# Performance work log

Hardware: AMD Instinct MI355X
Metric: run time of the kernel (lower is better)

## Reference

```python
import jax, jax.numpy as jnp
import numpy as np

B, N, D, H = 1, 512, 128, 128  # batch, seq, pair dim, hidden dim
EPS = 1e-6  # flax nnx LayerNorm default epsilon


def _layernorm(x, scale, bias):
    m = jnp.mean(x, axis=-1, keepdims=True)
    v = jnp.var(x, axis=-1, keepdims=True)
    return (x - m) * jax.lax.rsqrt(v + EPS) * scale + bias


def setup_inputs() -> dict:
    key = jax.random.key(0)
    ks = jax.random.split(key, 12)
    s = 0.02  # param init scale
    inp = {
        "x": jax.random.normal(ks[0], (B, N, N, D), jnp.float32),
        "src_mask": jnp.ones((B, N), jnp.float32),
        # first LayerNorm
        "ln1_scale": jnp.ones((D,), jnp.float32),
        "ln1_bias": jnp.zeros((D,), jnp.float32),
        # left/right projections
        "wl": jax.random.normal(ks[1], (D, H), jnp.float32) * s,
        "bl": jnp.zeros((H,), jnp.float32),
        "wr": jax.random.normal(ks[2], (D, H), jnp.float32) * s,
        "br": jnp.zeros((H,), jnp.float32),
        # gates (original inits kernel=0, bias=1; use small random kernels + bias=1 for a nontrivial baseline)
        "wlg": jax.random.normal(ks[3], (D, H), jnp.float32) * s,
        "blg": jnp.ones((H,), jnp.float32),
        "wrg": jax.random.normal(ks[4], (D, H), jnp.float32) * s,
        "brg": jnp.ones((H,), jnp.float32),
        "wog": jax.random.normal(ks[5], (D, H), jnp.float32) * s,
        "bog": jnp.ones((H,), jnp.float32),
        # output LayerNorm + projection
        "ln2_scale": jnp.ones((H,), jnp.float32),
        "ln2_bias": jnp.zeros((H,), jnp.float32),
        "wo": jax.random.normal(ks[6], (H, D), jnp.float32) * s,
        "bo": jnp.zeros((D,), jnp.float32),
    }
    return inp


def reference(x, src_mask, ln1_scale, ln1_bias, wl, bl, wr, br, wlg, blg,
              wrg, brg, wog, bog, ln2_scale, ln2_bias, wo, bo):
    # mask[b,i,j] = src_mask[b,i] * src_mask[b,j]  -> [B,N,N,1]
    sm = src_mask.astype(jnp.float32)
    mask = (sm[:, :, None] * sm[:, None, :])[..., None]

    xn = _layernorm(x, ln1_scale, ln1_bias)  # [B,N,N,D]

    # projections, mask, gates (gating after transpose in the original is
    # elementwise, hence equivalent applied pre-transpose)
    left = (xn @ wl + bl) * mask * jax.nn.sigmoid(xn @ wlg + blg)   # [B,N,N,H]
    right = (xn @ wr + br) * mask * jax.nn.sigmoid(xn @ wrg + brg)  # [B,N,N,H]
    out_gate = jax.nn.sigmoid(xn @ wog + bog)                       # [B,N,N,H]

    # 'ingoing' mix: out[b,i,j,d] = sum_k left[b,k,i,d] * right[b,k,j,d]
    out = jnp.einsum('bkid,bkjd->bijd', left, right)

    out = _layernorm(out, ln2_scale, ln2_bias) * out_gate
    return out @ wo + bo
```

## Files before the change

kernel.cpp:

```cpp
#include <hip/hip_runtime.h>
#include <hip/hip_bf16.h>


#define NSEQ 512
#define NN 262144
#define PL 262400
#define DMODEL 128

typedef __attribute__((ext_vector_type(8))) short short8;
typedef __attribute__((ext_vector_type(4))) float f32x4;

__device__ __forceinline__ unsigned short f2b(float f) {
    __hip_bfloat16 h = __float2bfloat16(f);
    return *reinterpret_cast<unsigned short*>(&h);
}
__device__ __forceinline__ float b2f(unsigned short u) {
    __hip_bfloat16 h;
    *reinterpret_cast<unsigned short*>(&h) = u;
    return __bfloat162float(h);
}
__device__ __forceinline__ unsigned int cvt_pk_bf16(float lo, float hi) {
    unsigned int r;
    asm("v_cvt_pk_bf16_f32 %0, %1, %2" : "=v"(r) : "v"(lo), "v"(hi));
    return r;
}
__device__ __forceinline__ float sigfast(float x) {
    return __builtin_amdgcn_rcpf(1.f + __builtin_amdgcn_exp2f(x * -1.44269504f));
}
__device__ __forceinline__ void gload_lds16(const void* g, void* l) {
    __builtin_amdgcn_global_load_lds(
        (const __attribute__((address_space(1))) void*)g,
        (__attribute__((address_space(3))) void*)l, 16, 0, 0);
}

__global__ __launch_bounds__(256) void k_wt_all(
    const float* __restrict__ w0, const float* __restrict__ w1,
    const float* __restrict__ w2, const float* __restrict__ w3,
    const float* __restrict__ w4, const float* __restrict__ w5,
    unsigned short* __restrict__ wt) {
    int bid = blockIdx.x;
    int mat = bid >> 6;
    const float* w = (mat == 0) ? w0 : (mat == 1) ? w1 : (mat == 2) ? w2
                   : (mat == 3) ? w3 : (mat == 4) ? w4 : w5;
    int idx = (bid & 63) * 256 + threadIdx.x;
    int d = idx >> 7, h = idx & 127;
    wt[mat * 16384 + h * 128 + d] = f2b(w[idx]);
}

__global__ __launch_bounds__(256) void k_ln1(const float* __restrict__ x,
                                             const float* __restrict__ sc,
                                             const float* __restrict__ bi,
                                             unsigned short* __restrict__ xn) {
    int t = threadIdx.x;
    int l = t & 31;
    size_t row = (size_t)blockIdx.x * 8 + (t >> 5);
    float4 v = *(const float4*)(x + row * DMODEL + l * 4);
    float s  = v.x + v.y + v.z + v.w;
    float sq = v.x * v.x + v.y * v.y + v.z * v.z + v.w * v.w;
    #pragma unroll
    for (int m = 1; m < 32; m <<= 1) {
        s  += __shfl_xor(s, m);
        sq += __shfl_xor(sq, m);
    }
    float mean = s * (1.f / 128.f);
    float var  = sq * (1.f / 128.f) - mean * mean;
    float inv  = rsqrtf(var + 1e-6f);
    float4 scv = *(const float4*)(sc + l * 4);
    float4 biv = *(const float4*)(bi + l * 4);
    uint2 pk;
    pk.x = cvt_pk_bf16((v.x - mean) * inv * scv.x + biv.x,
                       (v.y - mean) * inv * scv.y + biv.y);
    pk.y = cvt_pk_bf16((v.z - mean) * inv * scv.z + biv.z,
                       (v.w - mean) * inv * scv.w + biv.w);
    *(uint2*)(xn + row * DMODEL + l * 4) = pk;
}

__global__ __launch_bounds__(256, 2) void k_proj(
    const unsigned short* __restrict__ xn,
    const float* __restrict__ src_mask,
    const unsigned short* __restrict__ wt,
    const float* __restrict__ bl,  const float* __restrict__ blg,
    const float* __restrict__ br,  const float* __restrict__ brg,
    const float* __restrict__ bog,
    unsigned short* __restrict__ left_t,
    unsigned short* __restrict__ right_t,
    unsigned short* __restrict__ og) {
    __shared__ __align__(16) unsigned short As[64 * 136];
    const int t = threadIdx.x;
    const int lane = t & 63;
    const int wv = t >> 6;
    const int a0 = blockIdx.x * 64;
    const int b  = blockIdx.y;
    const int n0 = wv * 32;

    short8 bfA[2][4], bfB[2][4];
    auto loadB = [&](short8 (&dst)[2][4], int mat) {
        const unsigned short* base = wt + mat * 16384 + (lane >> 4) * 8;
        #pragma unroll
        for (int nf = 0; nf < 2; ++nf)
            #pragma unroll
            for (int kc = 0; kc < 4; ++kc)
                dst[nf][kc] = *(const short8*)(
                    base + (n0 + nf * 16 + (lane & 15)) * 128 + kc * 32);
    };
    loadB(bfA, 0);
    loadB(bfB, 1);

    #pragma unroll
    for (int it = 0; it < 4; ++it) {
        int idx = it * 256 + t;
        int row = idx >> 4, c = idx & 15;
        *(short8*)(&As[row * 136 + c * 8]) =
            *(const short8*)(xn + ((size_t)(a0 + row) * NSEQ + b) * DMODEL + c * 8);
    }
    __syncthreads();

    short8 af[4][4];
    #pragma unroll
    for (int mf = 0; mf < 4; ++mf)
        #pragma unroll
        for (int kc = 0; kc < 4; ++kc)
            af[mf][kc] = *(const short8*)(
                &As[(mf * 16 + (lane & 15)) * 136 + kc * 32 + (lane >> 4) * 8]);

    f32x4 acc0[4][2], acc1[4][2];
    float smb = src_mask[b];

    auto mmat = [&](f32x4 (&acc)[4][2], short8 (&bf)[2][4]) {
        #pragma unroll
        for (int mf = 0; mf < 4; ++mf)
            #pragma unroll
            for (int nf = 0; nf < 2; ++nf)
                acc[mf][nf] = f32x4{0.f, 0.f, 0.f, 0.f};
        #pragma unroll
        for (int kc = 0; kc < 4; ++kc)
            #pragma unroll
            for (int mf = 0; mf < 4; ++mf)
                #pragma unroll
                for (int nf = 0; nf < 2; ++nf)
                    acc[mf][nf] = __builtin_amdgcn_mfma_f32_16x16x32_bf16(
                        af[mf][kc], bf[nf][kc], acc[mf][nf], 0, 0, 0);
    };
    auto epi_pair = [&](const float* b1, const float* b2, unsigned short* dst) {
        float mkv[16];
        #pragma unroll
        for (int mf = 0; mf < 4; ++mf)
            #pragma unroll
            for (int j = 0; j < 4; ++j)
                mkv[mf * 4 + j] =
                    src_mask[a0 + mf * 16 + ((lane >> 4) << 2) + j] * smb;
        #pragma unroll
        for (int nf = 0; nf < 2; ++nf) {
            int h = n0 + nf * 16 + (lane & 15);
            float b1v = b1[h], b2v = b2[h];
            #pragma unroll
            for (int mf = 0; mf < 4; ++mf) {
                int abase = a0 + mf * 16 + ((lane >> 4) << 2);
                float o_[4];
                #pragma unroll
                for (int j = 0; j < 4; ++j) {
                    float pv = acc0[mf][nf][j] + b1v;
                    float gv = acc1[mf][nf][j] + b2v;
                    o_[j] = pv * mkv[mf * 4 + j] * sigfast(gv);
                }
                uint2 pk;
                pk.x = cvt_pk_bf16(o_[0], o_[1]);
                pk.y = cvt_pk_bf16(o_[2], o_[3]);
                *(uint2*)(dst + (size_t)h * PL + (size_t)b * NSEQ + abase) = pk;
            }
        }
    };

    mmat(acc0, bfA);
    loadB(bfA, 2);
    mmat(acc1, bfB);
    loadB(bfB, 3);
    epi_pair(bl, blg, left_t);
    mmat(acc0, bfA);
    loadB(bfA, 4);
    mmat(acc1, bfB);
    epi_pair(br, brg, right_t);
    mmat(acc0, bfA);

    __syncthreads();
    #pragma unroll
    for (int nf = 0; nf < 2; ++nf) {
        int h = n0 + nf * 16 + (lane & 15);
        float bv = bog[h];
        #pragma unroll
        for (int mf = 0; mf < 4; ++mf) {
            int rloc = mf * 16 + ((lane >> 4) << 2);
            #pragma unroll
            for (int j = 0; j < 4; ++j)
                As[(rloc + j) * 136 + h] = f2b(sigfast(acc0[mf][nf][j] + bv));
        }
    }
    __syncthreads();
    #pragma unroll
    for (int it = 0; it < 4; ++it) {
        int idx = it * 256 + t;
        int row = idx >> 4, c = idx & 15;
        *(short8*)(og + ((size_t)(a0 + row) * NSEQ + b) * DMODEL + c * 8) =
            *(const short8*)(&As[row * 136 + c * 8]);
    }
}

__global__ __launch_bounds__(256) void k_einsum(
    const unsigned short* __restrict__ lt,
    const unsigned short* __restrict__ rt,
    unsigned short* __restrict__ mid) {
    __shared__ __align__(16) unsigned short As[2][128 * 32];
    __shared__ __align__(16) unsigned short Bs[2][128 * 32];
    const int t = threadIdx.x, lane = t & 63, wv = t >> 6;
    const int bid = blockIdx.x;
    const int xcd = bid & 7, slot = bid >> 3;
    const int d = xcd * 16 + (slot >> 4);
    const int tile = slot & 15;
    const int i0 = (tile >> 2) * 128, j0 = (tile & 3) * 128;
    const int m0 = (wv >> 1) * 64, n0 = (wv & 1) * 64;
    const unsigned short* Ag = lt + (size_t)d * PL;
    const unsigned short* Bg = rt + (size_t)d * PL;

    auto stage = [&](int buf, int k0) {
        #pragma unroll
        for (int r = 0; r < 2; ++r) {
            int c = r * 256 + wv * 64 + lane;
            int row = c >> 2, sub = c & 3;
            gload_lds16(Ag + (size_t)(i0 + row) * NSEQ + k0 + sub * 8,
                        &As[buf][(r * 256 + wv * 64) * 8]);
            gload_lds16(Bg + (size_t)(j0 + row) * NSEQ + k0 + sub * 8,
                        &Bs[buf][(r * 256 + wv * 64) * 8]);
        }
    };

    f32x4 acc[4][4];
    #pragma unroll
    for (int mf = 0; mf < 4; ++mf)
        #pragma unroll
        for (int nf = 0; nf < 4; ++nf)
            acc[mf][nf] = f32x4{0.f, 0.f, 0.f, 0.f};

    stage(0, 0);
    int cur = 0;
    const int ko = (lane >> 4) * 8;
    for (int it = 0; it < 16; ++it) {
        __syncthreads();
        if (it < 15) stage(cur ^ 1, (it + 1) * 32);
        short8 af[4], bf[4];
        #pragma unroll
        for (int mf = 0; mf < 4; ++mf)
            af[mf] = *(const short8*)(&As[cur][(m0 + mf * 16 + (lane & 15)) * 32 + ko]);
        #pragma unroll
        for (int nf = 0; nf < 4; ++nf)
            bf[nf] = *(const short8*)(&Bs[cur][(n0 + nf * 16 + (lane & 15)) * 32 + ko]);
        #pragma unroll
        for (int mf = 0; mf < 4; ++mf)
            #pragma unroll
            for (int nf = 0; nf < 4; ++nf)
                acc[mf][nf] = __builtin_amdgcn_mfma_f32_16x16x32_bf16(
                    af[mf], bf[nf], acc[mf][nf], 0, 0, 0);
        cur ^= 1;
    }
    unsigned short* out = mid + (size_t)d * PL;
    #pragma unroll
    for (int mf = 0; mf < 4; ++mf) {
        int rbase = i0 + m0 + mf * 16 + ((lane >> 4) << 2);
        #pragma unroll
        for (int nf = 0; nf < 4; ++nf) {
            int col = j0 + n0 + nf * 16 + (lane & 15);
            #pragma unroll
            for (int j = 0; j < 4; ++j)
                out[(size_t)(rbase + j) * NSEQ + col] = f2b(acc[mf][nf][j]);
        }
    }
}

__global__ __launch_bounds__(256) void k_lnout(
    const unsigned short* __restrict__ mid,
    const unsigned short* __restrict__ og,
    const float* __restrict__ sc, const float* __restrict__ bi,
    const unsigned short* __restrict__ wt_o,
    const float* __restrict__ bo,
    float* __restrict__ out) {
    __shared__ __align__(16) unsigned short As[64 * 136];
    __shared__ __align__(16) unsigned short Bs[128 * 136];
    __shared__ float2 st[4][64];
    const int t = threadIdx.x, lane = t & 63, wv = t >> 6;
    const size_t p0 = (size_t)blockIdx.x * 64;
    const size_t p = p0 + lane;
    const int d0 = wv * 32;

    #pragma unroll
    for (int it = 0; it < 8; ++it) {
        int idx = it * 256 + t;
        int h = idx >> 4, c = idx & 15;
        *(short8*)(&Bs[h * 136 + c * 8]) = *(const short8*)(wt_o + h * 128 + c * 8);
    }

    unsigned short v16[32];
    float s = 0.f, sq = 0.f;
    #pragma unroll
    for (int e = 0; e < 32; ++e) {
        unsigned short u = mid[(size_t)(d0 + e) * PL + p];
        v16[e] = u;
        float f = b2f(u);
        s += f; sq += f * f;
    }
    st[wv][lane] = float2{s, sq};
    __syncthreads();
    float2 s0 = st[0][lane], s1 = st[1][lane], s2 = st[2][lane], s3 = st[3][lane];
    float S = s0.x + s1.x + s2.x + s3.x;
    float Q = s0.y + s1.y + s2.y + s3.y;
    float mean = S * (1.f / 128.f);
    float inv  = rsqrtf(Q * (1.f / 128.f) - mean * mean + 1e-6f);

    #pragma unroll
    for (int c = 0; c < 4; ++c) {
        short8 ov = *(const short8*)(og + p * DMODEL + d0 + c * 8);
        float y[8];
        #pragma unroll
        for (int e = 0; e < 8; ++e) {
            int dd = d0 + c * 8 + e;
            float v = b2f(v16[c * 8 + e]);
            y[e] = ((v - mean) * inv * sc[dd] + bi[dd]) * b2f((unsigned short)ov[e]);
        }
        uint4 pk;
        pk.x = cvt_pk_bf16(y[0], y[1]);
        pk.y = cvt_pk_bf16(y[2], y[3]);
        pk.z = cvt_pk_bf16(y[4], y[5]);
        pk.w = cvt_pk_bf16(y[6], y[7]);
        *(uint4*)(&As[lane * 136 + d0 + c * 8]) = pk;
    }
    __syncthreads();

    const int n0 = wv * 32;
    f32x4 acc[4][2];
    #pragma unroll
    for (int mf = 0; mf < 4; ++mf)
        #pragma unroll
        for (int nf = 0; nf < 2; ++nf)
            acc[mf][nf] = f32x4{0.f, 0.f, 0.f, 0.f};
    #pragma unroll
    for (int kc = 0; kc < 4; ++kc) {
        int ko = kc * 32 + (lane >> 4) * 8;
        short8 af[4], bf[2];
        #pragma unroll
        for (int mf = 0; mf < 4; ++mf)
            af[mf] = *(const short8*)(&As[(mf * 16 + (lane & 15)) * 136 + ko]);
        #pragma unroll
        for (int nf = 0; nf < 2; ++nf)
            bf[nf] = *(const short8*)(&Bs[(n0 + nf * 16 + (lane & 15)) * 136 + ko]);
        #pragma unroll
        for (int mf = 0; mf < 4; ++mf)
            #pragma unroll
            for (int nf = 0; nf < 2; ++nf)
                acc[mf][nf] = __builtin_amdgcn_mfma_f32_16x16x32_bf16(
                    af[mf], bf[nf], acc[mf][nf], 0, 0, 0);
    }
    #pragma unroll
    for (int nf = 0; nf < 2; ++nf) {
        int n = n0 + nf * 16 + (lane & 15);
        float bv = bo[n];
        #pragma unroll
        for (int mf = 0; mf < 4; ++mf) {
            int rb = mf * 16 + ((lane >> 4) << 2);
            #pragma unroll
            for (int j = 0; j < 4; ++j)
                out[(p0 + rb + j) * DMODEL + n] = acc[mf][nf][j] + bv;
        }
    }
}

extern "C" void kernel_launch(void* const* d_in, const int* in_sizes, int n_in,
                              void* d_out, int out_size, void* d_ws, size_t ws_size,
                              hipStream_t stream) {
    const float* x    = (const float*)d_in[0];
    const float* sm   = (const float*)d_in[1];
    const float* ln1s = (const float*)d_in[2];
    const float* ln1b = (const float*)d_in[3];
    const float* wl   = (const float*)d_in[4];
    const float* bl   = (const float*)d_in[5];
    const float* wr   = (const float*)d_in[6];
    const float* br   = (const float*)d_in[7];
    const float* wlg  = (const float*)d_in[8];
    const float* blg  = (const float*)d_in[9];
    const float* wrg  = (const float*)d_in[10];
    const float* brg  = (const float*)d_in[11];
    const float* wog  = (const float*)d_in[12];
    const float* bog  = (const float*)d_in[13];
    const float* ln2s = (const float*)d_in[14];
    const float* ln2b = (const float*)d_in[15];
    const float* wo   = (const float*)d_in[16];
    const float* bo   = (const float*)d_in[17];
    float* out = (float*)d_out;

    char* ws = (char*)d_ws;
    const size_t SZ_XN = 67108864ull;
    const size_t SZ_PL = (size_t)PL * 128 * 2;
    unsigned short* wt  = (unsigned short*)ws;
    unsigned short* xn  = (unsigned short*)(ws + 196608);
    unsigned short* lt  = (unsigned short*)(ws + 196608 + SZ_XN);
    unsigned short* rt  = (unsigned short*)(ws + 196608 + SZ_XN + SZ_PL);
    unsigned short* ogb = (unsigned short*)(ws + 196608 + SZ_XN + 2 * SZ_PL);
    unsigned short* mid = (unsigned short*)(ws + 196608 + 2 * SZ_XN + 2 * SZ_PL);

    k_wt_all<<<384, 256, 0, stream>>>(wl, wlg, wr, wrg, wog, wo, wt);
    k_ln1<<<32768, 256, 0, stream>>>(x, ln1s, ln1b, xn);
    k_proj<<<dim3(8, 512), 256, 0, stream>>>(xn, sm, wt,
                                             bl, blg, br, brg, bog, lt, rt, ogb);
    k_einsum<<<2048, 256, 0, stream>>>(lt, rt, mid);
    k_lnout<<<4096, 256, 0, stream>>>(mid, ogb, ln2s, ln2b,
                                      wt + 5 * 16384, bo, out);
}
```

Before: 295.8 us.

## Compute output gate inside LN-out kernel from xn instead of materializing it

Removes the output-gate projection from the projection kernel and recomputes it with MFMA inside the final LayerNorm/output kernel, reading xn directly and staging the sigmoid gate in shared memory. This eliminates writing and re-reading a 64 MB bf16 gate tensor. The cost is an extra xn read in k_lnout, more shared memory per block (possibly lower occupancy), and some extra matrix work in that kernel.

```diff
diff --git a/kernel.cpp b/kernel.cpp
--- a/kernel.cpp
+++ b/kernel.cpp
@@ -81,10 +81,8 @@
     const unsigned short* __restrict__ wt,
     const float* __restrict__ bl,  const float* __restrict__ blg,
     const float* __restrict__ br,  const float* __restrict__ brg,
-    const float* __restrict__ bog,
     unsigned short* __restrict__ left_t,
-    unsigned short* __restrict__ right_t,
-    unsigned short* __restrict__ og) {
+    unsigned short* __restrict__ right_t) {
     __shared__ __align__(16) unsigned short As[64 * 136];
     const int t = threadIdx.x;
     const int lane = t & 63;
@@ -177,32 +175,8 @@
     loadB(bfB, 3);
     epi_pair(bl, blg, left_t);
     mmat(acc0, bfA);
-    loadB(bfA, 4);
     mmat(acc1, bfB);
     epi_pair(br, brg, right_t);
-    mmat(acc0, bfA);
-
-    __syncthreads();
-    #pragma unroll
-    for (int nf = 0; nf < 2; ++nf) {
-        int h = n0 + nf * 16 + (lane & 15);
-        float bv = bog[h];
-        #pragma unroll
-        for (int mf = 0; mf < 4; ++mf) {
-            int rloc = mf * 16 + ((lane >> 4) << 2);
-            #pragma unroll
-            for (int j = 0; j < 4; ++j)
-                As[(rloc + j) * 136 + h] = f2b(sigfast(acc0[mf][nf][j] + bv));
-        }
-    }
-    __syncthreads();
-    #pragma unroll
-    for (int it = 0; it < 4; ++it) {
-        int idx = it * 256 + t;
-        int row = idx >> 4, c = idx & 15;
-        *(short8*)(og + ((size_t)(a0 + row) * NSEQ + b) * DMODEL + c * 8) =
-            *(const short8*)(&As[row * 136 + c * 8]);
-    }
 }
 
 __global__ __launch_bounds__(256) void k_einsum(
@@ -277,13 +251,16 @@
 
 __global__ __launch_bounds__(256) void k_lnout(
     const unsigned short* __restrict__ mid,
-    const unsigned short* __restrict__ og,
+    const unsigned short* __restrict__ xn,
+    const unsigned short* __restrict__ wg,
+    const float* __restrict__ bog,
     const float* __restrict__ sc, const float* __restrict__ bi,
     const unsigned short* __restrict__ wt_o,
     const float* __restrict__ bo,
     float* __restrict__ out) {
     __shared__ __align__(16) unsigned short As[64 * 136];
     __shared__ __align__(16) unsigned short Bs[128 * 136];
+    __shared__ __align__(16) unsigned short Og[64 * 132];
     __shared__ float2 st[4][64];
     const int t = threadIdx.x, lane = t & 63, wv = t >> 6;
     const size_t p0 = (size_t)blockIdx.x * 64;
@@ -297,6 +274,31 @@
         *(short8*)(&Bs[h * 136 + c * 8]) = *(const short8*)(wt_o + h * 128 + c * 8);
     }
 
+    f32x4 ga[4][2];
+    #pragma unroll
+    for (int mf = 0; mf < 4; ++mf)
+        #pragma unroll
+        for (int nf = 0; nf < 2; ++nf)
+            ga[mf][nf] = f32x4{0.f, 0.f, 0.f, 0.f};
+    #pragma unroll
+    for (int kc = 0; kc < 4; ++kc) {
+        short8 af[4], gb[2];
+        #pragma unroll
+        for (int mf = 0; mf < 4; ++mf)
+            af[mf] = *(const short8*)(
+                xn + (p0 + mf * 16 + (lane & 15)) * DMODEL + kc * 32 + (lane >> 4) * 8);
+        #pragma unroll
+        for (int nf = 0; nf < 2; ++nf)
+            gb[nf] = *(const short8*)(
+                wg + (d0 + nf * 16 + (lane & 15)) * 128 + kc * 32 + (lane >> 4) * 8);
+        #pragma unroll
+        for (int mf = 0; mf < 4; ++mf)
+            #pragma unroll
+            for (int nf = 0; nf < 2; ++nf)
+                ga[mf][nf] = __builtin_amdgcn_mfma_f32_16x16x32_bf16(
+                    af[mf], gb[nf], ga[mf][nf], 0, 0, 0);
+    }
+
     unsigned short v16[32];
     float s = 0.f, sq = 0.f;
     #pragma unroll
@@ -306,6 +308,20 @@
         float f = b2f(u);
         s += f; sq += f * f;
     }
+
+    #pragma unroll
+    for (int nf = 0; nf < 2; ++nf) {
+        int hc = d0 + nf * 16 + (lane & 15);
+        float bv = bog[hc];
+        #pragma unroll
+        for (int mf = 0; mf < 4; ++mf) {
+            int r = mf * 16 + ((lane >> 4) << 2);
+            #pragma unroll
+            for (int j = 0; j < 4; ++j)
+                Og[(r + j) * 132 + hc] = f2b(sigfast(ga[mf][nf][j] + bv));
+        }
+    }
+
     st[wv][lane] = float2{s, sq};
     __syncthreads();
     float2 s0 = st[0][lane], s1 = st[1][lane], s2 = st[2][lane], s3 = st[3][lane];
@@ -316,7 +332,7 @@
 
     #pragma unroll
     for (int c = 0; c < 4; ++c) {
-        short8 ov = *(const short8*)(og + p * DMODEL + d0 + c * 8);
+        short8 ov = *(const short8*)(&Og[lane * 132 + d0 + c * 8]);
         float y[8];
         #pragma unroll
         for (int e = 0; e < 8; ++e) {
@@ -401,14 +417,13 @@
     unsigned short* xn  = (unsigned short*)(ws + 196608);
     unsigned short* lt  = (unsigned short*)(ws + 196608 + SZ_XN);
     unsigned short* rt  = (unsigned short*)(ws + 196608 + SZ_XN + SZ_PL);
-    unsigned short* ogb = (unsigned short*)(ws + 196608 + SZ_XN + 2 * SZ_PL);
-    unsigned short* mid = (unsigned short*)(ws + 196608 + 2 * SZ_XN + 2 * SZ_PL);
+    unsigned short* mid = (unsigned short*)(ws + 196608 + SZ_XN + 2 * SZ_PL);
 
     k_wt_all<<<384, 256, 0, stream>>>(wl, wlg, wr, wrg, wog, wo, wt);
     k_ln1<<<32768, 256, 0, stream>>>(x, ln1s, ln1b, xn);
     k_proj<<<dim3(8, 512), 256, 0, stream>>>(xn, sm, wt,
-                                             bl, blg, br, brg, bog, lt, rt, ogb);
+                                             bl, blg, br, brg, lt, rt);
     k_einsum<<<2048, 256, 0, stream>>>(lt, rt, mid);
-    k_lnout<<<4096, 256, 0, stream>>>(mid, ogb, ln2s, ln2b,
-                                      wt + 5 * 16384, bo, out);
-}
+    k_lnout<<<4096, 256, 0, stream>>>(mid, xn, wt + 4 * 16384, bog,
+                                      ln2s, ln2b, wt + 5 * 16384, bo, out);
+}
```

Result: no change. 301.3 us (+1.9%).
